# Optimization experiments

Hardware: AMD Instinct MI355X
Metric: run time of the kernel (lower is better)

The kernel has to match this reference:

```python
import jax, jax.numpy as jnp
import numpy as np

B, T = 2048, 8
IN_DIM, OUT_DIM, E = 1024, 4096, 12


def setup_inputs() -> dict:
    key = jax.random.key(0)
    k = jax.random.split(key, 6)
    s = 1.0 / np.sqrt(IN_DIM)
    sg = 1.0 / np.sqrt(OUT_DIM)
    return {
        "x": jax.random.normal(k[0], (B, 1, IN_DIM), dtype=jnp.float32),
        "t": jax.random.normal(k[1], (B, T, OUT_DIM), dtype=jnp.float32),
        "W": jax.random.uniform(k[2], (E, IN_DIM, OUT_DIM), dtype=jnp.float32, minval=-s, maxval=s),
        "b": jax.random.uniform(k[3], (E, OUT_DIM), dtype=jnp.float32, minval=-s, maxval=s),
        "Wg": jax.random.uniform(k[4], (OUT_DIM, E), dtype=jnp.float32, minval=-sg, maxval=sg),
        "bg": jax.random.uniform(k[5], (E,), dtype=jnp.float32, minval=-sg, maxval=sg),
    }


def reference(x, t, W, b, Wg, bg):
    # x: [B,1,in], t: [B,T,out], W: [E,in,out], b: [E,out], Wg: [out,E], bg: [E]
    x_flat = x[:, 0, :]                                   # [B,in]
    t_mean = t.mean(axis=1)                               # [B,out]
    gate_logits = t_mean @ Wg + bg                        # [B,E]
    top1 = jnp.argmax(gate_logits, axis=-1)               # [B]
    # Dense per-expert linear, then select the top-1 expert's row per token.
    all_out = jnp.einsum('bi,eio->beo', x_flat, W) + b    # [B,E,out]
    out = all_out[jnp.arange(x.shape[0]), top1]           # [B,out]
    return out[:, None, :]                                # [B,1,out]
```

## Files before the change

### kernel.cpp

```cpp
#include <hip/hip_runtime.h>
#include <hip/hip_bf16.h>

#define B_ROWS  2048
#define T_DIM   8
#define IN_DIM  1024
#define OUT_DIM 4096
#define NE      12

#define M_TILE 128
#define N_TILE 128
#define K_STEP 32
#define NSTEP  (IN_DIM / K_STEP)
#define PACK_TILES 2
#define NCB    (OUT_DIM / N_TILE)

typedef __attribute__((ext_vector_type(8))) short short8;
typedef __attribute__((ext_vector_type(4))) float f32x4;

union S8U { short8 s; unsigned u[4]; };

__device__ __forceinline__ unsigned cvt2(float a, float b) {
  __hip_bfloat162 h = __float22bfloat162_rn(make_float2(a, b));
  union { __hip_bfloat162 h; unsigned u; } c; c.h = h;
  return c.u;
}

__device__ __forceinline__ void barrier_lgkm() {
  asm volatile("s_waitcnt lgkmcnt(0)" ::: "memory");
  __builtin_amdgcn_s_barrier();
}

__device__ __forceinline__ void gload_lds16(const void* g, void* l) {
  __builtin_amdgcn_global_load_lds(
      (const __attribute__((address_space(1))) void*)g,
      (__attribute__((address_space(3))) void*)l, 16, 0, 0);
}

__global__ __launch_bounds__(256) void wg_transpose(
    const float* __restrict__ Wg, float* __restrict__ wgt)
{
  const int c = blockIdx.x * 256 + threadIdx.x;
  #pragma unroll
  for (int e = 0; e < NE; ++e)
    wgt[(size_t)e * OUT_DIM + c] = Wg[(size_t)c * NE + e];
}

__global__ __launch_bounds__(256) void gate_kernel(
    const float* __restrict__ t, const float* __restrict__ wgt,
    const float* __restrict__ bg, int* __restrict__ counts,
    int* __restrict__ rowlist)
{
  const int b   = blockIdx.x;
  const int tid = threadIdx.x;
  const float* tb = t + (size_t)b * T_DIM * OUT_DIM;

  float4 m[4];
  #pragma unroll
  for (int it = 0; it < 4; ++it) {
    const int c = (tid + it * 256) * 4;
    float4 s = make_float4(0.f, 0.f, 0.f, 0.f);
    #pragma unroll
    for (int tt = 0; tt < T_DIM; ++tt) {
      const float4 v = *(const float4*)(tb + (size_t)tt * OUT_DIM + c);
      s.x += v.x; s.y += v.y; s.z += v.z; s.w += v.w;
    }
    m[it] = make_float4(s.x * 0.125f, s.y * 0.125f, s.z * 0.125f, s.w * 0.125f);
  }

  float part[NE];
  #pragma unroll
  for (int e = 0; e < NE; ++e) {
    float acc = 0.f;
    #pragma unroll
    for (int it = 0; it < 4; ++it) {
      const int c = (tid + it * 256) * 4;
      const float4 w = *(const float4*)(wgt + (size_t)e * OUT_DIM + c);
      acc += m[it].x * w.x; acc += m[it].y * w.y;
      acc += m[it].z * w.z; acc += m[it].w * w.w;
    }
    part[e] = acc;
  }

  double d[NE];
  #pragma unroll
  for (int e = 0; e < NE; ++e) d[e] = (double)part[e];
  #pragma unroll
  for (int off = 32; off > 0; off >>= 1) {
    #pragma unroll
    for (int e = 0; e < NE; ++e) d[e] += __shfl_down(d[e], off, 64);
  }

  __shared__ double wsred[4][NE];
  const int lane = tid & 63, wave = tid >> 6;
  if (lane == 0) {
    #pragma unroll
    for (int e = 0; e < NE; ++e) wsred[wave][e] = d[e];
  }
  __syncthreads();

  if (tid == 0) {
    double best = -1e300; int bi = 0;
    #pragma unroll
    for (int e = 0; e < NE; ++e) {
      const double v = wsred[0][e] + wsred[1][e] + wsred[2][e] + wsred[3][e] + (double)bg[e];
      if (v > best) { best = v; bi = e; }
    }
    const int pos = atomicAdd(&counts[bi], 1);
    rowlist[bi * B_ROWS + pos] = b;
  }
}

__global__ __launch_bounds__(256) void gate_fallback(
    const float* __restrict__ t, const float* __restrict__ Wg,
    const float* __restrict__ bg, int* __restrict__ counts,
    int* __restrict__ rowlist)
{
  const int b   = blockIdx.x;
  const int tid = threadIdx.x;
  const float* tb = t + (size_t)b * T_DIM * OUT_DIM;

  float part[NE];
  #pragma unroll
  for (int e = 0; e < NE; ++e) part[e] = 0.f;
  #pragma unroll
  for (int it = 0; it < 4; ++it) {
    const int c = (tid + it * 256) * 4;
    float4 s = make_float4(0.f, 0.f, 0.f, 0.f);
    #pragma unroll
    for (int tt = 0; tt < T_DIM; ++tt) {
      const float4 v = *(const float4*)(tb + (size_t)tt * OUT_DIM + c);
      s.x += v.x; s.y += v.y; s.z += v.z; s.w += v.w;
    }
    const float mm[4] = { s.x * 0.125f, s.y * 0.125f, s.z * 0.125f, s.w * 0.125f };
    #pragma unroll
    for (int j = 0; j < 4; ++j) {
      const float* wg = Wg + (size_t)(c + j) * NE;
      #pragma unroll
      for (int e = 0; e < NE; ++e) part[e] += mm[j] * wg[e];
    }
  }
  double d[NE];
  #pragma unroll
  for (int e = 0; e < NE; ++e) d[e] = (double)part[e];
  #pragma unroll
  for (int off = 32; off > 0; off >>= 1) {
    #pragma unroll
    for (int e = 0; e < NE; ++e) d[e] += __shfl_down(d[e], off, 64);
  }
  __shared__ double wsred[4][NE];
  const int lane = tid & 63, wave = tid >> 6;
  if (lane == 0) {
    #pragma unroll
    for (int e = 0; e < NE; ++e) wsred[wave][e] = d[e];
  }
  __syncthreads();
  if (tid == 0) {
    double best = -1e300; int bi = 0;
    #pragma unroll
    for (int e = 0; e < NE; ++e) {
      const double v = wsred[0][e] + wsred[1][e] + wsred[2][e] + wsred[3][e] + (double)bg[e];
      if (v > best) { best = v; bi = e; }
    }
    const int pos = atomicAdd(&counts[bi], 1);
    rowlist[bi * B_ROWS + pos] = b;
  }
}

__global__ __launch_bounds__(256) void pack_x(
    const float* __restrict__ x, const int* __restrict__ counts,
    const int* __restrict__ rowlist, short8* __restrict__ pxa)
{
  const int e   = blockIdx.x;
  const int rt  = blockIdx.y;
  const int it  = blockIdx.z;
  const int cnt = counts[e];
  const int row0 = rt * M_TILE;
  if (row0 >= cnt) return;
  const int* rl = rowlist + e * B_ROWS;
  const int tid = threadIdx.x;
  const int sg = (tid >> 4) & 3, slr = tid & 15, smb = tid >> 6;

  int g0 = row0 + smb * 16 + slr;        g0 = g0 < cnt ? g0 : cnt - 1;
  int g1 = row0 + (smb + 4) * 16 + slr;  g1 = g1 < cnt ? g1 : cnt - 1;
  const float* xp0 = x + (size_t)rl[g0] * IN_DIM + sg * 8 + it * K_STEP;
  const float* xp1 = x + (size_t)rl[g1] * IN_DIM + sg * 8 + it * K_STEP;

  const float4 a = *(const float4*)xp0, b = *(const float4*)(xp0 + 4);
  const float4 c = *(const float4*)xp1, d = *(const float4*)(xp1 + 4);
  S8U v0, v1;
  v0.u[0] = cvt2(a.x, a.y); v0.u[1] = cvt2(a.z, a.w);
  v0.u[2] = cvt2(b.x, b.y); v0.u[3] = cvt2(b.z, b.w);
  v1.u[0] = cvt2(c.x, c.y); v1.u[1] = cvt2(c.z, c.w);
  v1.u[2] = cvt2(d.x, d.y); v1.u[3] = cvt2(d.z, d.w);

  short8* dst = pxa + ((size_t)(e * PACK_TILES + rt) * NSTEP + it) * 512;
  dst[tid]       = v0.s;
  dst[tid + 256] = v1.s;
}

__global__ __launch_bounds__(512) void expert_gemm8(
    const float* __restrict__ W, const float* __restrict__ bias,
    const int* __restrict__ counts, const int* __restrict__ rowlist,
    const short8* __restrict__ pxa, float* __restrict__ out)
{
  const int bid = blockIdx.x;
  const int wk  = (bid & 7) * 48 + (bid >> 3);
  const int e   = wk >> 5;
  const int cb  = wk & 31;
  const int cnt = counts[e];
  const int c0  = cb * N_TILE;
  const int* rl = rowlist + e * B_ROWS;

  __shared__ short8 xa[2][1024];
  __shared__ short8 wb[2][512];

  const int tid  = threadIdx.x;
  const int lane = tid & 63;
  const int wave = tid >> 6;

  const int sg = (tid >> 4) & 3, slr = tid & 15, smb = tid >> 6;
  const float* wp = W + (size_t)e * IN_DIM * OUT_DIM
                      + (size_t)(sg * 8) * OUT_DIM + c0 + smb * 16 + slr;

  const short8* at = pxa + (size_t)(e * PACK_TILES + (wave >> 2)) * NSTEP * 512
                   + (wave & 3) * 128 + lane;

  const int wm = (wave >> 1) * 64;
  const int wn = (wave & 1) * 64;
  const int abase = (wave >> 2) * 512 + ((wave >> 1) & 1) * 256;
  const int bbase = (wave & 1) * 256;

  f32x4 acc[4][4];
  #pragma unroll
  for (int m = 0; m < 4; ++m)
    #pragma unroll
    for (int n = 0; n < 4; ++n)
      #pragma unroll
      for (int q = 0; q < 4; ++q) acc[m][n][q] = 0.f;

  float w0[8];

#define W_ISSUE(K)                                                      \
  {                                                                     \
    const float* p = wp + (size_t)(K) * OUT_DIM;                        \
    _Pragma("unroll")                                                   \
    for (int j = 0; j < 8; ++j) w0[j] = p[(size_t)j * OUT_DIM];         \
  }
#define A_DMA(IT, BUF)                                                  \
  {                                                                     \
    gload_lds16(at + (size_t)(IT) * 512,      &xa[BUF][wave * 128]);    \
    gload_lds16(at + (size_t)(IT) * 512 + 64, &xa[BUF][wave * 128 + 64]); \
    __builtin_amdgcn_sched_barrier(0);                                  \
  }

  W_ISSUE(0);
  A_DMA(0, 0);

  for (int it = 0; it < NSTEP; ++it) {
    const int buf = it & 1;
    const int itn = (it + 1) & (NSTEP - 1);

    S8U bv;
    #pragma unroll
    for (int q = 0; q < 4; ++q)
      bv.u[q] = cvt2(w0[2 * q], w0[2 * q + 1]);

    W_ISSUE(itn * K_STEP);
    wb[buf][tid] = bv.s;

    asm volatile("s_waitcnt vmcnt(8) lgkmcnt(0)" ::: "memory");
    __builtin_amdgcn_s_barrier();

    A_DMA(itn, buf ^ 1);

    short8 af[4], bf[4];
    #pragma unroll
    for (int m = 0; m < 4; ++m) af[m] = xa[buf][abase + m * 64 + lane];
    #pragma unroll
    for (int n = 0; n < 4; ++n) bf[n] = wb[buf][bbase + n * 64 + lane];
    #pragma unroll
    for (int m = 0; m < 4; ++m)
      #pragma unroll
      for (int n = 0; n < 4; ++n)
        acc[m][n] = __builtin_amdgcn_mfma_f32_16x16x32_bf16(af[m], bf[n], acc[m][n], 0, 0, 0);
  }
#undef W_ISSUE
#undef A_DMA

  const int lr = lane & 15;
  const int lq = (lane >> 4) * 4;
  float bcol[4];
  #pragma unroll
  for (int n = 0; n < 4; ++n)
    bcol[n] = bias[e * OUT_DIM + c0 + wn + n * 16 + lr];

  #pragma unroll
  for (int m = 0; m < 4; ++m) {
    #pragma unroll
    for (int r = 0; r < 4; ++r) {
      const int gidx = wm + m * 16 + lq + r;
      if (gidx >= cnt) continue;
      const int grow = rl[gidx];
      float* orow = out + (size_t)grow * OUT_DIM;
      #pragma unroll
      for (int n = 0; n < 4; ++n) {
        const int col = c0 + wn + n * 16 + lr;
        orow[col] = acc[m][n][r] + bcol[n];
      }
    }
  }
}

__global__ __launch_bounds__(256) void expert_gemm_legacy(
    const float* __restrict__ x, const float* __restrict__ W,
    const float* __restrict__ bias, const int* __restrict__ counts,
    const int* __restrict__ rowlist, float* __restrict__ out, int y_off)
{
  const int e    = blockIdx.z;
  const int cnt  = counts[e];
  const int row0 = (blockIdx.y + y_off) * M_TILE;
  if (row0 >= cnt) return;
  const int c0   = blockIdx.x * N_TILE;
  const int* rl  = rowlist + e * B_ROWS;

  __shared__ short8 xa[2][512];
  __shared__ short8 wb[2][512];

  const int tid  = threadIdx.x;
  const int lane = tid & 63;
  const int wave = tid >> 6;
  const int sg  = (tid >> 4) & 3;
  const int slr = tid & 15;
  const int smb = tid >> 6;

  int arow0, arow1;
  {
    const int g0 = row0 + smb * 16 + slr;
    const int g1 = row0 + (smb + 4) * 16 + slr;
    arow0 = rl[g0 < cnt ? g0 : cnt - 1];
    arow1 = rl[g1 < cnt ? g1 : cnt - 1];
  }
  const float* xp0 = x + (size_t)arow0 * IN_DIM + sg * 8;
  const float* xp1 = x + (size_t)arow1 * IN_DIM + sg * 8;
  const float* wp  = W + (size_t)e * IN_DIM * OUT_DIM
                       + (size_t)(sg * 8) * OUT_DIM + c0 + smb * 16 + slr;

  const int wm = (wave >> 1) * 64;
  const int wn = (wave & 1) * 64;
  const int abase = (wave >> 1) * 256;
  const int bbase = (wave & 1) * 256;

  f32x4 acc[4][4];
  #pragma unroll
  for (int m = 0; m < 4; ++m)
    #pragma unroll
    for (int n = 0; n < 4; ++n)
      #pragma unroll
      for (int q = 0; q < 4; ++q) acc[m][n][q] = 0.f;

  float4 a0lo, a0hi, a1lo, a1hi;
  float w0[8], w1[8];

#define ISSUE_LOADS(K)                                                  \
  {                                                                     \
    a0lo = *(const float4*)(xp0 + (K));                                 \
    a0hi = *(const float4*)(xp0 + (K) + 4);                             \
    a1lo = *(const float4*)(xp1 + (K));                                 \
    a1hi = *(const float4*)(xp1 + (K) + 4);                             \
    const float* p = wp + (size_t)(K) * OUT_DIM;                        \
    _Pragma("unroll")                                                   \
    for (int j = 0; j < 8; ++j) {                                       \
      w0[j] = p[(size_t)j * OUT_DIM];                                   \
      w1[j] = p[(size_t)j * OUT_DIM + 64];                              \
    }                                                                   \
  }

  ISSUE_LOADS(0);

  for (int it = 0; it < NSTEP; ++it) {
    S8U av0, av1, bv0, bv1;
    av0.u[0] = cvt2(a0lo.x, a0lo.y); av0.u[1] = cvt2(a0lo.z, a0lo.w);
    av0.u[2] = cvt2(a0hi.x, a0hi.y); av0.u[3] = cvt2(a0hi.z, a0hi.w);
    av1.u[0] = cvt2(a1lo.x, a1lo.y); av1.u[1] = cvt2(a1lo.z, a1lo.w);
    av1.u[2] = cvt2(a1hi.x, a1hi.y); av1.u[3] = cvt2(a1hi.z, a1hi.w);
    #pragma unroll
    for (int q = 0; q < 4; ++q) {
      bv0.u[q] = cvt2(w0[2 * q], w0[2 * q + 1]);
      bv1.u[q] = cvt2(w1[2 * q], w1[2 * q + 1]);
    }

    if (it + 1 < NSTEP) ISSUE_LOADS((it + 1) * K_STEP);

    const int buf = it & 1;
    xa[buf][tid]       = av0.s;
    xa[buf][tid + 256] = av1.s;
    wb[buf][tid]       = bv0.s;
    wb[buf][tid + 256] = bv1.s;
    barrier_lgkm();

    short8 af[4], bf[4];
    #pragma unroll
    for (int m = 0; m < 4; ++m) af[m] = xa[buf][abase + m * 64 + lane];
    #pragma unroll
    for (int n = 0; n < 4; ++n) bf[n] = wb[buf][bbase + n * 64 + lane];
    #pragma unroll
    for (int m = 0; m < 4; ++m)
      #pragma unroll
      for (int n = 0; n < 4; ++n)
        acc[m][n] = __builtin_amdgcn_mfma_f32_16x16x32_bf16(af[m], bf[n], acc[m][n], 0, 0, 0);
  }
#undef ISSUE_LOADS

  const int lr = lane & 15;
  const int lq = (lane >> 4) * 4;
  float bcol[4];
  #pragma unroll
  for (int n = 0; n < 4; ++n)
    bcol[n] = bias[e * OUT_DIM + c0 + wn + n * 16 + lr];

  #pragma unroll
  for (int m = 0; m < 4; ++m) {
    #pragma unroll
    for (int r = 0; r < 4; ++r) {
      const int gidx = row0 + wm + m * 16 + lq + r;
      if (gidx >= cnt) continue;
      const int grow = rl[gidx];
      float* orow = out + (size_t)grow * OUT_DIM;
      #pragma unroll
      for (int n = 0; n < 4; ++n) {
        const int col = c0 + wn + n * 16 + lr;
        orow[col] = acc[m][n][r] + bcol[n];
      }
    }
  }
}

extern "C" void kernel_launch(void* const* d_in, const int* in_sizes, int n_in,
                              void* d_out, int out_size, void* d_ws, size_t ws_size,
                              hipStream_t stream) {
  (void)in_sizes; (void)n_in; (void)out_size;
  const float* x  = (const float*)d_in[0];
  const float* t  = (const float*)d_in[1];
  const float* W  = (const float*)d_in[2];
  const float* bb = (const float*)d_in[3];
  const float* Wg = (const float*)d_in[4];
  const float* bg = (const float*)d_in[5];
  float* out = (float*)d_out;

  char*  base    = (char*)d_ws;
  int*   counts  = (int*)base;
  int*   rowlist = (int*)(base + 64);
  float* wgt     = (float*)(base + 98368);
  short8* pxa    = (short8*)(base + 295936);
  const size_t need_wgt  = 294976;
  const size_t need_pack = 295936 + (size_t)NE * PACK_TILES * NSTEP * 512 * 16;

  hipMemsetAsync(counts, 0, 64, stream);
  if (ws_size >= need_wgt) {
    wg_transpose<<<OUT_DIM / 256, 256, 0, stream>>>(Wg, wgt);
    gate_kernel<<<B_ROWS, 256, 0, stream>>>(t, wgt, bg, counts, rowlist);
  } else {
    gate_fallback<<<B_ROWS, 256, 0, stream>>>(t, Wg, bg, counts, rowlist);
  }

  if (ws_size >= need_pack) {
    pack_x<<<dim3(NE, PACK_TILES, NSTEP), 256, 0, stream>>>(x, counts, rowlist, pxa);
    expert_gemm8<<<dim3(NE * NCB, 1, 1), 512, 0, stream>>>(
        W, bb, counts, rowlist, pxa, out);
    expert_gemm_legacy<<<dim3(NCB, B_ROWS / M_TILE - PACK_TILES, NE),
                         256, 0, stream>>>(x, W, bb, counts, rowlist, out, PACK_TILES);
  } else {
    expert_gemm_legacy<<<dim3(NCB, B_ROWS / M_TILE, NE),
                         256, 0, stream>>>(x, W, bb, counts, rowlist, out, 0);
  }
}
```

Before: 140.8 us.

## Narrow expert GEMM tile to 64 columns with 4 waves and double-buffered W loads

Rewrites the main expert GEMM from 512-thread blocks covering 256x128 to 256-thread blocks covering 256x64, doubling the block count to 768 for better CU occupancy and load spread. W prefetch is now issued two K-steps ahead using two alternating register sets, giving more latency hiding for the strided fp32 weight reads. Each wave now owns 64 rows across all 64 columns. The trade-off is that every row tile of A is loaded from LDS twice as often per output column, and each block does more A DMA relative to its compute.

```diff
diff --git a/kernel.cpp b/kernel.cpp
--- a/kernel.cpp
+++ b/kernel.cpp
@@ -13,6 +13,7 @@
 #define NSTEP  (IN_DIM / K_STEP)
 #define PACK_TILES 2
 #define NCB    (OUT_DIM / N_TILE)
+#define NCB4   (OUT_DIM / 64)
 
 typedef __attribute__((ext_vector_type(8))) short short8;
 typedef __attribute__((ext_vector_type(4))) float f32x4;
@@ -198,37 +199,32 @@
   dst[tid + 256] = v1.s;
 }
 
-__global__ __launch_bounds__(512) void expert_gemm8(
+__global__ __launch_bounds__(256) void expert_gemm4(
     const float* __restrict__ W, const float* __restrict__ bias,
     const int* __restrict__ counts, const int* __restrict__ rowlist,
     const short8* __restrict__ pxa, float* __restrict__ out)
 {
   const int bid = blockIdx.x;
-  const int wk  = (bid & 7) * 48 + (bid >> 3);
-  const int e   = wk >> 5;
-  const int cb  = wk & 31;
+  const int wk  = (bid & 7) * 96 + (bid >> 3);
+  const int e   = wk >> 6;
+  const int cb  = wk & 63;
   const int cnt = counts[e];
-  const int c0  = cb * N_TILE;
+  const int c0  = cb * 64;
   const int* rl = rowlist + e * B_ROWS;
 
   __shared__ short8 xa[2][1024];
-  __shared__ short8 wb[2][512];
+  __shared__ short8 wb[2][256];
 
   const int tid  = threadIdx.x;
   const int lane = tid & 63;
   const int wave = tid >> 6;
 
-  const int sg = (tid >> 4) & 3, slr = tid & 15, smb = tid >> 6;
+  const int g = (tid >> 4) & 3, lc = tid & 15, nb = tid >> 6;
   const float* wp = W + (size_t)e * IN_DIM * OUT_DIM
-                      + (size_t)(sg * 8) * OUT_DIM + c0 + smb * 16 + slr;
-
-  const short8* at = pxa + (size_t)(e * PACK_TILES + (wave >> 2)) * NSTEP * 512
-                   + (wave & 3) * 128 + lane;
-
-  const int wm = (wave >> 1) * 64;
-  const int wn = (wave & 1) * 64;
-  const int abase = (wave >> 2) * 512 + ((wave >> 1) & 1) * 256;
-  const int bbase = (wave & 1) * 256;
+                      + (size_t)(g * 8) * OUT_DIM + c0 + nb * 16 + lc;
+
+  const short8* at = pxa + (size_t)(e * PACK_TILES + (wave >> 1)) * NSTEP * 512
+                   + (wave & 1) * 256 + lane;
 
   f32x4 acc[4][4];
   #pragma unroll
@@ -238,73 +234,81 @@
       #pragma unroll
       for (int q = 0; q < 4; ++q) acc[m][n][q] = 0.f;
 
-  float w0[8];
-
-#define W_ISSUE(K)                                                      \
+  float wA[8], wB[8];
+
+#define W_ISSUE(SET, K)                                                 \
   {                                                                     \
     const float* p = wp + (size_t)(K) * OUT_DIM;                        \
     _Pragma("unroll")                                                   \
-    for (int j = 0; j < 8; ++j) w0[j] = p[(size_t)j * OUT_DIM];         \
+    for (int j = 0; j < 8; ++j) w##SET[j] = p[(size_t)j * OUT_DIM];     \
   }
 #define A_DMA(IT, BUF)                                                  \
   {                                                                     \
-    gload_lds16(at + (size_t)(IT) * 512,      &xa[BUF][wave * 128]);    \
-    gload_lds16(at + (size_t)(IT) * 512 + 64, &xa[BUF][wave * 128 + 64]); \
+    gload_lds16(at + (size_t)(IT) * 512,       &xa[BUF][wave * 256]);       \
+    gload_lds16(at + (size_t)(IT) * 512 + 64,  &xa[BUF][wave * 256 + 64]);  \
+    gload_lds16(at + (size_t)(IT) * 512 + 128, &xa[BUF][wave * 256 + 128]); \
+    gload_lds16(at + (size_t)(IT) * 512 + 192, &xa[BUF][wave * 256 + 192]); \
     __builtin_amdgcn_sched_barrier(0);                                  \
   }
-
-  W_ISSUE(0);
+#define GEMM_STEP(SET, IT)                                              \
+  {                                                                     \
+    const int buf = (IT) & 1;                                           \
+    S8U bv;                                                             \
+    _Pragma("unroll")                                                   \
+    for (int q = 0; q < 4; ++q)                                         \
+      bv.u[q] = cvt2(w##SET[2 * q], w##SET[2 * q + 1]);                 \
+    wb[buf][tid] = bv.s;                                                \
+    asm volatile("s_waitcnt vmcnt(8) lgkmcnt(0)" ::: "memory");         \
+    __builtin_amdgcn_s_barrier();                                       \
+    A_DMA(((IT) + 1) & (NSTEP - 1), buf ^ 1);                           \
+    W_ISSUE(SET, (((IT) + 2) & (NSTEP - 1)) * K_STEP);                  \
+    __builtin_amdgcn_sched_barrier(0);                                  \
+    short8 af[4], bf[4];                                                \
+    _Pragma("unroll")                                                   \
+    for (int m = 0; m < 4; ++m)                                         \
+      af[m] = xa[buf][wave * 256 + m * 64 + lane];                      \
+    _Pragma("unroll")                                                   \
+    for (int n = 0; n < 4; ++n)                                         \
+      bf[n] = wb[buf][n * 64 + lane];                                   \
+    _Pragma("unroll")                                                   \
+    for (int m = 0; m < 4; ++m)                                         \
+      _Pragma("unroll")                                                 \
+      for (int n = 0; n < 4; ++n)                                       \
+        acc[m][n] = __builtin_amdgcn_mfma_f32_16x16x32_bf16(            \
+            af[m], bf[n], acc[m][n], 0, 0, 0);                          \
+  }
+
   A_DMA(0, 0);
-
-  for (int it = 0; it < NSTEP; ++it) {
-    const int buf = it & 1;
-    const int itn = (it + 1) & (NSTEP - 1);
-
-    S8U bv;
-    #pragma unroll
-    for (int q = 0; q < 4; ++q)
-      bv.u[q] = cvt2(w0[2 * q], w0[2 * q + 1]);
-
-    W_ISSUE(itn * K_STEP);
-    wb[buf][tid] = bv.s;
-
-    asm volatile("s_waitcnt vmcnt(8) lgkmcnt(0)" ::: "memory");
-    __builtin_amdgcn_s_barrier();
-
-    A_DMA(itn, buf ^ 1);
-
-    short8 af[4], bf[4];
-    #pragma unroll
-    for (int m = 0; m < 4; ++m) af[m] = xa[buf][abase + m * 64 + lane];
-    #pragma unroll
-    for (int n = 0; n < 4; ++n) bf[n] = wb[buf][bbase + n * 64 + lane];
-    #pragma unroll
-    for (int m = 0; m < 4; ++m)
-      #pragma unroll
-      for (int n = 0; n < 4; ++n)
-        acc[m][n] = __builtin_amdgcn_mfma_f32_16x16x32_bf16(af[m], bf[n], acc[m][n], 0, 0, 0);
-  }
+  W_ISSUE(A, 0);
+  W_ISSUE(B, K_STEP);
+  __builtin_amdgcn_sched_barrier(0);
+
+  for (int it = 0; it < NSTEP; it += 2) {
+    GEMM_STEP(A, it);
+    GEMM_STEP(B, it + 1);
+  }
+#undef GEMM_STEP
+#undef A_DMA
 #undef W_ISSUE
-#undef A_DMA
 
   const int lr = lane & 15;
   const int lq = (lane >> 4) * 4;
   float bcol[4];
   #pragma unroll
   for (int n = 0; n < 4; ++n)
-    bcol[n] = bias[e * OUT_DIM + c0 + wn + n * 16 + lr];
+    bcol[n] = bias[e * OUT_DIM + c0 + n * 16 + lr];
 
   #pragma unroll
   for (int m = 0; m < 4; ++m) {
     #pragma unroll
     for (int r = 0; r < 4; ++r) {
-      const int gidx = wm + m * 16 + lq + r;
+      const int gidx = wave * 64 + m * 16 + lq + r;
       if (gidx >= cnt) continue;
       const int grow = rl[gidx];
       float* orow = out + (size_t)grow * OUT_DIM;
       #pragma unroll
       for (int n = 0; n < 4; ++n) {
-        const int col = c0 + wn + n * 16 + lr;
+        const int col = c0 + n * 16 + lr;
         orow[col] = acc[m][n][r] + bcol[n];
       }
     }
@@ -465,7 +469,7 @@
 
   if (ws_size >= need_pack) {
     pack_x<<<dim3(NE, PACK_TILES, NSTEP), 256, 0, stream>>>(x, counts, rowlist, pxa);
-    expert_gemm8<<<dim3(NE * NCB, 1, 1), 512, 0, stream>>>(
+    expert_gemm4<<<dim3(NE * NCB4, 1, 1), 256, 0, stream>>>(
         W, bb, counts, rowlist, pxa, out);
     expert_gemm_legacy<<<dim3(NCB, B_ROWS / M_TILE - PACK_TILES, NE),
                          256, 0, stream>>>(x, W, bb, counts, rowlist, out, PACK_TILES);
```

Result: slower. 165.0 us (+17.2%).

## Widen expert GEMM N tile to 256 columns per block

Applied to the files above, without the earlier changes.

The packed expert GEMM now has each 512-thread block cover 256 output columns instead of 128, halving the grid to 192 blocks. Every block loads and converts two W strips per K step and keeps a 4x8 accumulator array per wave, so each A fragment read from LDS feeds twice as many MFMAs and the packed x tiles are re-streamed half as often. In exchange the kernel uses more registers and LDS, which can lower occupancy, and with only 192 blocks the device is less fully loaded.

```diff
diff --git a/kernel.cpp b/kernel.cpp
--- a/kernel.cpp
+++ b/kernel.cpp
@@ -13,6 +13,7 @@
 #define NSTEP  (IN_DIM / K_STEP)
 #define PACK_TILES 2
 #define NCB    (OUT_DIM / N_TILE)
+#define NCB16  (OUT_DIM / 256)
 
 typedef __attribute__((ext_vector_type(8))) short short8;
 typedef __attribute__((ext_vector_type(4))) float f32x4;
@@ -198,53 +199,56 @@
   dst[tid + 256] = v1.s;
 }
 
-__global__ __launch_bounds__(512) void expert_gemm8(
+__global__ __launch_bounds__(512) void expert_gemm16(
     const float* __restrict__ W, const float* __restrict__ bias,
     const int* __restrict__ counts, const int* __restrict__ rowlist,
     const short8* __restrict__ pxa, float* __restrict__ out)
 {
   const int bid = blockIdx.x;
-  const int wk  = (bid & 7) * 48 + (bid >> 3);
-  const int e   = wk >> 5;
-  const int cb  = wk & 31;
+  const int wk  = (bid & 7) * 24 + (bid >> 3);
+  const int e   = wk >> 4;
+  const int cb  = wk & 15;
   const int cnt = counts[e];
-  const int c0  = cb * N_TILE;
+  const int c0  = cb * 256;
   const int* rl = rowlist + e * B_ROWS;
 
   __shared__ short8 xa[2][1024];
-  __shared__ short8 wb[2][512];
+  __shared__ short8 wb[2][1024];
 
   const int tid  = threadIdx.x;
   const int lane = tid & 63;
   const int wave = tid >> 6;
 
-  const int sg = (tid >> 4) & 3, slr = tid & 15, smb = tid >> 6;
+  const int g = (tid >> 4) & 3, lc = tid & 15, nb = tid >> 6;
   const float* wp = W + (size_t)e * IN_DIM * OUT_DIM
-                      + (size_t)(sg * 8) * OUT_DIM + c0 + smb * 16 + slr;
+                      + (size_t)(g * 8) * OUT_DIM + c0 + nb * 16 + lc;
 
   const short8* at = pxa + (size_t)(e * PACK_TILES + (wave >> 2)) * NSTEP * 512
                    + (wave & 3) * 128 + lane;
 
   const int wm = (wave >> 1) * 64;
-  const int wn = (wave & 1) * 64;
-  const int abase = (wave >> 2) * 512 + ((wave >> 1) & 1) * 256;
-  const int bbase = (wave & 1) * 256;
-
-  f32x4 acc[4][4];
+  const int wn = (wave & 1) * 128;
+  const int abase = wm * 4;
+  const int bbase = wn * 4;
+
+  f32x4 acc[4][8];
   #pragma unroll
   for (int m = 0; m < 4; ++m)
     #pragma unroll
-    for (int n = 0; n < 4; ++n)
+    for (int n = 0; n < 8; ++n)
       #pragma unroll
       for (int q = 0; q < 4; ++q) acc[m][n][q] = 0.f;
 
-  float w0[8];
+  float w0[8], w1[8];
 
 #define W_ISSUE(K)                                                      \
   {                                                                     \
     const float* p = wp + (size_t)(K) * OUT_DIM;                        \
     _Pragma("unroll")                                                   \
-    for (int j = 0; j < 8; ++j) w0[j] = p[(size_t)j * OUT_DIM];         \
+    for (int j = 0; j < 8; ++j) {                                       \
+      w0[j] = p[(size_t)j * OUT_DIM];                                   \
+      w1[j] = p[(size_t)j * OUT_DIM + 128];                             \
+    }                                                                   \
   }
 #define A_DMA(IT, BUF)                                                  \
   {                                                                     \
@@ -260,28 +264,31 @@
     const int buf = it & 1;
     const int itn = (it + 1) & (NSTEP - 1);
 
-    S8U bv;
-    #pragma unroll
-    for (int q = 0; q < 4; ++q)
-      bv.u[q] = cvt2(w0[2 * q], w0[2 * q + 1]);
+    S8U bv0, bv1;
+    #pragma unroll
+    for (int q = 0; q < 4; ++q) {
+      bv0.u[q] = cvt2(w0[2 * q], w0[2 * q + 1]);
+      bv1.u[q] = cvt2(w1[2 * q], w1[2 * q + 1]);
+    }
 
     W_ISSUE(itn * K_STEP);
-    wb[buf][tid] = bv.s;
-
-    asm volatile("s_waitcnt vmcnt(8) lgkmcnt(0)" ::: "memory");
+    wb[buf][tid]       = bv0.s;
+    wb[buf][tid + 512] = bv1.s;
+
+    asm volatile("s_waitcnt vmcnt(16) lgkmcnt(0)" ::: "memory");
     __builtin_amdgcn_s_barrier();
 
     A_DMA(itn, buf ^ 1);
 
-    short8 af[4], bf[4];
+    short8 af[4], bf[8];
     #pragma unroll
     for (int m = 0; m < 4; ++m) af[m] = xa[buf][abase + m * 64 + lane];
     #pragma unroll
-    for (int n = 0; n < 4; ++n) bf[n] = wb[buf][bbase + n * 64 + lane];
+    for (int n = 0; n < 8; ++n) bf[n] = wb[buf][bbase + n * 64 + lane];
     #pragma unroll
     for (int m = 0; m < 4; ++m)
       #pragma unroll
-      for (int n = 0; n < 4; ++n)
+      for (int n = 0; n < 8; ++n)
         acc[m][n] = __builtin_amdgcn_mfma_f32_16x16x32_bf16(af[m], bf[n], acc[m][n], 0, 0, 0);
   }
 #undef W_ISSUE
@@ -289,9 +296,9 @@
 
   const int lr = lane & 15;
   const int lq = (lane >> 4) * 4;
-  float bcol[4];
-  #pragma unroll
-  for (int n = 0; n < 4; ++n)
+  float bcol[8];
+  #pragma unroll
+  for (int n = 0; n < 8; ++n)
     bcol[n] = bias[e * OUT_DIM + c0 + wn + n * 16 + lr];
 
   #pragma unroll
@@ -303,7 +310,7 @@
       const int grow = rl[gidx];
       float* orow = out + (size_t)grow * OUT_DIM;
       #pragma unroll
-      for (int n = 0; n < 4; ++n) {
+      for (int n = 0; n < 8; ++n) {
         const int col = c0 + wn + n * 16 + lr;
         orow[col] = acc[m][n][r] + bcol[n];
       }
@@ -465,7 +472,7 @@
 
   if (ws_size >= need_pack) {
     pack_x<<<dim3(NE, PACK_TILES, NSTEP), 256, 0, stream>>>(x, counts, rowlist, pxa);
-    expert_gemm8<<<dim3(NE * NCB, 1, 1), 512, 0, stream>>>(
+    expert_gemm16<<<dim3(NE * NCB16, 1, 1), 512, 0, stream>>>(
         W, bb, counts, rowlist, pxa, out);
     expert_gemm_legacy<<<dim3(NCB, B_ROWS / M_TILE - PACK_TILES, NE),
                          256, 0, stream>>>(x, W, bb, counts, rowlist, out, PACK_TILES);
```

Result: slower. 151.7 us (+7.8%).
